# Performance work log

Measured on AMD Instinct MI355X. Metric: run time of the kernel, lower is better.

## Reference

```python
import jax, jax.numpy as jnp
import numpy as np

N, D = 16384, 4096  # anchors x candidates


def setup_inputs() -> dict:
    key = jax.random.key(0)
    k1, k2 = jax.random.split(key)
    labels = jax.random.normal(k1, (N, D), dtype=jnp.float32)
    logits = jax.random.normal(k2, (N, D), dtype=jnp.float32)
    mask = jnp.ones((N, D), dtype=jnp.bool_)  # accepted by the torch module but unused
    alpha = jnp.full((1,), 0.07, dtype=jnp.float32)  # temperature
    return {"labels": labels, "logits": logits, "mask": mask, "alpha": alpha}


def reference(labels, logits, mask, alpha):
    # logits / alpha, then cross-entropy against the argmax-of-labels column.
    # The torch code's masked_select + concat merely moves the positive column
    # to index 0 before CE with target 0 -- mathematically identical to this.
    scaled = logits / alpha  # [N, D]
    pos_idx = jnp.argmax(labels, axis=1)  # [N]
    logz = jax.nn.logsumexp(scaled, axis=1)  # [N], stable
    pos = jnp.take_along_axis(scaled, pos_idx[:, None], axis=1)[:, 0]  # [N]
    return jnp.mean(logz - pos)
```

## Files before the change

### kernel.cpp

```cpp
#include <hip/hip_runtime.h>
#include <math.h>


typedef float vf4 __attribute__((ext_vector_type(4)));

constexpr int Dk    = 4096;
constexpr int BLOCK = 256;

__global__ __launch_bounds__(BLOCK) void nce_main(
    const float* __restrict__ labels, const float* __restrict__ logits,
    const float* __restrict__ alpha, float* __restrict__ bins)
{
    const int row = blockIdx.x;
    const int t   = threadIdx.x;
    const size_t base = (size_t)row * Dk;
    const vf4* lab4 = reinterpret_cast<const vf4*>(labels + base);
    const vf4* lg4  = reinterpret_cast<const vf4*>(logits + base);

    vf4 g[4], l[4];
#pragma unroll
    for (int k = 0; k < 4; ++k)
        g[k] = __builtin_nontemporal_load(lg4 + t + k * BLOCK);
#pragma unroll
    for (int k = 0; k < 4; ++k)
        l[k] = __builtin_nontemporal_load(lab4 + t + k * BLOCK);

    const float inv_alpha = 1.0f / alpha[0];

    float m    = -INFINITY;
    float lmax = -INFINITY;
    int   lidx = 0x7fffffff;
    float lval = 0.0f;
#pragma unroll
    for (int k = 0; k < 4; ++k) {
#pragma unroll
        for (int e = 0; e < 4; ++e) {
            const float ge = g[k][e];
            const float le = l[k][e];
            m = fmaxf(m, ge);
            const int idx = 4 * (t + k * BLOCK) + e;
            if (le > lmax || (le == lmax && idx < lidx)) {
                lmax = le; lidx = idx; lval = ge;
            }
        }
    }

    __shared__ float s_m[BLOCK / 64];
#pragma unroll
    for (int off = 1; off < 64; off <<= 1)
        m = fmaxf(m, __shfl_xor(m, off));
    if ((t & 63) == 0) s_m[t >> 6] = m;
    __syncthreads();
    const float M = fmaxf(fmaxf(s_m[0], s_m[1]), fmaxf(s_m[2], s_m[3]));

    float s = 0.0f;
#pragma unroll
    for (int k = 0; k < 4; ++k) {
        s += __expf((g[k][0] - M) * inv_alpha);
        s += __expf((g[k][1] - M) * inv_alpha);
        s += __expf((g[k][2] - M) * inv_alpha);
        s += __expf((g[k][3] - M) * inv_alpha);
    }

#pragma unroll
    for (int off = 32; off; off >>= 1) {
        s += __shfl_down(s, off);
        const float om = __shfl_down(lmax, off);
        const int   oi = __shfl_down(lidx, off);
        const float ov = __shfl_down(lval, off);
        if (om > lmax || (om == lmax && oi < lidx)) { lmax = om; lidx = oi; lval = ov; }
    }

    __shared__ float s_s[BLOCK / 64], s_lm[BLOCK / 64], s_lv[BLOCK / 64];
    __shared__ int   s_li[BLOCK / 64];
    if ((t & 63) == 0) {
        const int w = t >> 6;
        s_s[w] = s; s_lm[w] = lmax; s_li[w] = lidx; s_lv[w] = lval;
    }
    __syncthreads();

    if (t == 0) {
        const float S = s_s[0] + s_s[1] + s_s[2] + s_s[3];
        float bm = s_lm[0]; int bi = s_li[0]; float bv = s_lv[0];
#pragma unroll
        for (int w = 1; w < 4; ++w) {
            if (s_lm[w] > bm || (s_lm[w] == bm && s_li[w] < bi)) {
                bm = s_lm[w]; bi = s_li[w]; bv = s_lv[w];
            }
        }
        bins[row] = (M - bv) * inv_alpha + logf(S);
    }
}

__global__ __launch_bounds__(BLOCK) void nce_finalize(
    const float* __restrict__ bins, float* __restrict__ out, int n, float inv_n)
{
    const int t = threadIdx.x;
    float v = 0.0f;
    for (int i = t; i < n; i += BLOCK) v += bins[i];
#pragma unroll
    for (int off = 32; off; off >>= 1) v += __shfl_down(v, off);
    __shared__ float s_w[BLOCK / 64];
    if ((t & 63) == 0) s_w[t >> 6] = v;
    __syncthreads();
    if (t == 0) out[0] = (s_w[0] + s_w[1] + s_w[2] + s_w[3]) * inv_n;
}

extern "C" void kernel_launch(void* const* d_in, const int* in_sizes, int n_in,
                              void* d_out, int out_size, void* d_ws, size_t ws_size,
                              hipStream_t stream) {
    const float* labels = (const float*)d_in[0];
    const float* logits = (const float*)d_in[1];
    const float* alpha  = (const float*)d_in[3];
    float* out  = (float*)d_out;
    float* bins = (float*)d_ws;

    const int N = in_sizes[0] / Dk;

    nce_main<<<N, BLOCK, 0, stream>>>(labels, logits, alpha, bins);
    nce_finalize<<<1, BLOCK, 0, stream>>>(bins, out, N, 1.0f / (float)N);
}
```

Measured before the change: 585.9 us.

## Assign one row per wavefront with online softmax, removing block barriers

Each wavefront now processes a full row, so reductions use only wave shuffles and the shared-memory exchanges and block barriers are gone. The max and sum-of-exponentials are fused into a single online pass over two halves of the row, with a running rescale. This is meant to cut synchronization stalls and let waves stream memory independently, at the cost of an extra exponential per four elements and a serial dependency on the running max.

```diff
diff --git a/kernel.cpp b/kernel.cpp
--- a/kernel.cpp
+++ b/kernel.cpp
@@ -6,61 +6,61 @@
 
 constexpr int Dk    = 4096;
 constexpr int BLOCK = 256;
+constexpr int ROWS_PER_BLOCK = 4;
 
 __global__ __launch_bounds__(BLOCK) void nce_main(
     const float* __restrict__ labels, const float* __restrict__ logits,
     const float* __restrict__ alpha, float* __restrict__ bins)
 {
-    const int row = blockIdx.x;
-    const int t   = threadIdx.x;
+    const int lane = threadIdx.x & 63;
+    const int wave = threadIdx.x >> 6;
+    const int row  = blockIdx.x * ROWS_PER_BLOCK + wave;
     const size_t base = (size_t)row * Dk;
-    const vf4* lab4 = reinterpret_cast<const vf4*>(labels + base);
-    const vf4* lg4  = reinterpret_cast<const vf4*>(logits + base);
+    const vf4* g4 = reinterpret_cast<const vf4*>(logits + base);
+    const vf4* l4 = reinterpret_cast<const vf4*>(labels + base);
+    const float ia = 1.0f / alpha[0];
 
-    vf4 g[4], l[4];
+    float m = -INFINITY, s = 0.0f;
+    float lmax = -INFINITY, lval = 0.0f;
+    int   lidx = 0x7fffffff;
+
+#pragma unroll 1
+    for (int half = 0; half < 2; ++half) {
+        const int c0 = half * 8;
+        vf4 g[8], l[8];
 #pragma unroll
-    for (int k = 0; k < 4; ++k)
-        g[k] = __builtin_nontemporal_load(lg4 + t + k * BLOCK);
+        for (int j = 0; j < 8; ++j)
+            g[j] = __builtin_nontemporal_load(g4 + lane + 64 * (c0 + j));
 #pragma unroll
-    for (int k = 0; k < 4; ++k)
-        l[k] = __builtin_nontemporal_load(lab4 + t + k * BLOCK);
+        for (int j = 0; j < 8; ++j)
+            l[j] = __builtin_nontemporal_load(l4 + lane + 64 * (c0 + j));
 
-    const float inv_alpha = 1.0f / alpha[0];
-
-    float m    = -INFINITY;
-    float lmax = -INFINITY;
-    int   lidx = 0x7fffffff;
-    float lval = 0.0f;
 #pragma unroll
-    for (int k = 0; k < 4; ++k) {
+        for (int j = 0; j < 8; ++j) {
+            const float c4 = fmaxf(fmaxf(g[j][0], g[j][1]), fmaxf(g[j][2], g[j][3]));
+            const float mn = fmaxf(m, c4);
+            const float e0 = __expf((g[j][0] - mn) * ia);
+            const float e1 = __expf((g[j][1] - mn) * ia);
+            const float e2 = __expf((g[j][2] - mn) * ia);
+            const float e3 = __expf((g[j][3] - mn) * ia);
+            s = s * __expf((m - mn) * ia) + ((e0 + e1) + (e2 + e3));
+            m = mn;
 #pragma unroll
-        for (int e = 0; e < 4; ++e) {
-            const float ge = g[k][e];
-            const float le = l[k][e];
-            m = fmaxf(m, ge);
-            const int idx = 4 * (t + k * BLOCK) + e;
-            if (le > lmax || (le == lmax && idx < lidx)) {
-                lmax = le; lidx = idx; lval = ge;
+            for (int e = 0; e < 4; ++e) {
+                const float le  = l[j][e];
+                const int   idx = 4 * (lane + 64 * (c0 + j)) + e;
+                if (le > lmax || (le == lmax && idx < lidx)) {
+                    lmax = le; lidx = idx; lval = g[j][e];
+                }
             }
         }
     }
 
-    __shared__ float s_m[BLOCK / 64];
+    float M = m;
 #pragma unroll
     for (int off = 1; off < 64; off <<= 1)
-        m = fmaxf(m, __shfl_xor(m, off));
-    if ((t & 63) == 0) s_m[t >> 6] = m;
-    __syncthreads();
-    const float M = fmaxf(fmaxf(s_m[0], s_m[1]), fmaxf(s_m[2], s_m[3]));
-
-    float s = 0.0f;
-#pragma unroll
-    for (int k = 0; k < 4; ++k) {
-        s += __expf((g[k][0] - M) * inv_alpha);
-        s += __expf((g[k][1] - M) * inv_alpha);
-        s += __expf((g[k][2] - M) * inv_alpha);
-        s += __expf((g[k][3] - M) * inv_alpha);
-    }
+        M = fmaxf(M, __shfl_xor(M, off));
+    s *= __expf((m - M) * ia);
 
 #pragma unroll
     for (int off = 32; off; off >>= 1) {
@@ -71,25 +71,8 @@
         if (om > lmax || (om == lmax && oi < lidx)) { lmax = om; lidx = oi; lval = ov; }
     }
 
-    __shared__ float s_s[BLOCK / 64], s_lm[BLOCK / 64], s_lv[BLOCK / 64];
-    __shared__ int   s_li[BLOCK / 64];
-    if ((t & 63) == 0) {
-        const int w = t >> 6;
-        s_s[w] = s; s_lm[w] = lmax; s_li[w] = lidx; s_lv[w] = lval;
-    }
-    __syncthreads();
-
-    if (t == 0) {
-        const float S = s_s[0] + s_s[1] + s_s[2] + s_s[3];
-        float bm = s_lm[0]; int bi = s_li[0]; float bv = s_lv[0];
-#pragma unroll
-        for (int w = 1; w < 4; ++w) {
-            if (s_lm[w] > bm || (s_lm[w] == bm && s_li[w] < bi)) {
-                bm = s_lm[w]; bi = s_li[w]; bv = s_lv[w];
-            }
-        }
-        bins[row] = (M - bv) * inv_alpha + logf(S);
-    }
+    if (lane == 0)
+        bins[row] = (M - lval) * ia + logf(s);
 }
 
 __global__ __launch_bounds__(BLOCK) void nce_finalize(
@@ -117,6 +100,6 @@
 
     const int N = in_sizes[0] / Dk;
 
-    nce_main<<<N, BLOCK, 0, stream>>>(labels, logits, alpha, bins);
+    nce_main<<<N / ROWS_PER_BLOCK, BLOCK, 0, stream>>>(labels, logits, alpha, bins);
     nce_finalize<<<1, BLOCK, 0, stream>>>(bins, out, N, 1.0f / (float)N);
 }
```

Result: no change. 589.6 us (+0.6%).
